# Optimization experiments

Measured on AMD Instinct MI355X. Metric: run time of the kernel, lower is better.

The kernel has to match this reference:

```python
import jax, jax.numpy as jnp
import numpy as np

LMAX = 3
D_IRREP = (LMAX + 1) ** 2  # 16
EPS = 1e-5


def _conv1d(x, w, pad):
    # x: [N, C_in, L], w: [C_out, C_in, K] -> [N, C_out, L]
    return jax.lax.conv_general_dilated(
        x, w, window_strides=(1,), padding=[(pad, pad)],
        dimension_numbers=("NCH", "OIH", "NCH"))


def setup_inputs() -> dict:
    key = jax.random.key(0)
    ks = jax.random.split(key, 8)
    B, Cin, Cout, N, K, RES = 128, 256, 256, 64, 5, 8
    return {
        "x": jax.random.normal(ks[0], (B, Cin * D_IRREP, N), jnp.float32),
        "weight": jax.random.normal(ks[1], (LMAX + 1, Cout, Cin, K), jnp.float32) / np.sqrt(Cin * K).astype(np.float32),
        "bias": jax.random.normal(ks[2], (1, 1, Cout), jnp.float32) * 0.02,
        "affine_weight": jnp.ones((LMAX + 1, Cout), jnp.float32),
        "gating_w": jax.random.normal(ks[3], (Cout, Cout), jnp.float32) / np.sqrt(Cout).astype(np.float32),
        "gating_b": jnp.zeros((Cout,), jnp.float32),
        "to_grid": jax.random.normal(ks[4], (RES, RES, D_IRREP), jnp.float32) * 0.3,
        "from_grid": jax.random.normal(ks[5], (RES, RES, D_IRREP), jnp.float32) * 0.3,
    }


def reference(x, weight, bias, affine_weight, gating_w, gating_b, to_grid, from_grid):
    B, CI, N = x.shape
    Cin = CI // D_IRREP
    Cout = weight.shape[1]
    pad = weight.shape[-1] // 2
    x = x.reshape(B, Cin, D_IRREP, N)

    # per-degree Conv1d over the time axis, irrep order folded into batch
    h_parts = []
    for l in range(LMAX + 1):
        lo, li = l * l, 2 * l + 1
        x_l = x[:, :, lo:lo + li, :]                                  # [B, Cin, li, N]
        x_l = x_l.transpose(0, 2, 1, 3).reshape(B * li, Cin, N)       # (b i) c n
        h_l = _conv1d(x_l, weight[l], pad)                            # [B*li, Cout, N]
        h_l = h_l.reshape(B, li, Cout, N).transpose(0, 3, 1, 2).reshape(B * N, li, Cout)  # (b n) i c
        if l == 0:
            h_l = h_l + bias
        h_parts.append(h_l)
    h = jnp.concatenate(h_parts, axis=1)                              # [B*N, 16, Cout]

    # rms_norm_sh: center l=0 over channels, degree-balanced RMS, per-degree affine
    degrees = np.repeat(np.arange(LMAX + 1), 2 * np.arange(LMAX + 1) + 1)  # [16]
    bal = jnp.asarray((1.0 / (2.0 * degrees + 1.0)) / (LMAX + 1), h.dtype)  # [16]
    mean0 = jnp.mean(h[:, :1, :], axis=2, keepdims=True)
    h = jnp.concatenate([h[:, :1, :] - mean0, h[:, 1:, :]], axis=1)
    var = jnp.einsum("zic,i->zc", h * h, bal)                         # [Z, C]
    inv = jax.lax.rsqrt(jnp.mean(var, axis=-1)[:, None, None] + EPS)  # [Z,1,1]
    h = h * inv * affine_weight[degrees][None]                        # [Z,16,C]

    # SeparableS2Activation: SiLU-gated scalars + S2 grid activation for l>0
    gate = jax.nn.silu(h[:, :1, :] @ gating_w.T + gating_b)           # [Z,1,C]
    grid = jax.nn.silu(jnp.einsum("bai,zic->zbac", to_grid, h))       # [Z,8,8,C]
    s2 = jnp.einsum("bai,zbac->zic", from_grid, grid)                 # [Z,16,C]
    h = jnp.concatenate([gate, s2[:, 1:, :]], axis=1)

    # (b n) i c -> b (c i) n
    out = h.reshape(B, N, D_IRREP, Cout).transpose(0, 3, 2, 1).reshape(B, Cout * D_IRREP, N)
    return out
```

## Files before the change

kernel.cpp:

```cpp
#include <hip/hip_runtime.h>
#include <hip/hip_bf16.h>

#define BB    128
#define CIN   256
#define COUT  256
#define NN    64
#define KW    5
#define DIRR  16
#define ZTOT  (BB*NN)
#define SX    264

typedef __attribute__((ext_vector_type(4))) float f32x4;
typedef __attribute__((ext_vector_type(8))) short s16x8;

__device__ inline ushort f2bf(float f) {
    __hip_bfloat16 h = __float2bfloat16(f);
    return *(const ushort*)&h;
}
__device__ inline float bf2f(ushort u) {
    union { unsigned int ui; float f; } cv; cv.ui = ((unsigned int)u) << 16;
    return cv.f;
}
__device__ inline float wave_sum(float v) {
    #pragma unroll
    for (int o = 32; o > 0; o >>= 1) v += __shfl_down(v, o, 64);
    return v;
}
__device__ inline float silu(float x) { return x / (1.f + __expf(-x)); }

__global__ __launch_bounds__(256) void pack_all_k(const float* __restrict__ w,
                                                  const float* __restrict__ gw,
                                                  const float* __restrict__ tg,
                                                  const float* __restrict__ fg,
                                                  ushort* __restrict__ wb,
                                                  ushort* __restrict__ gwb,
                                                  ushort* __restrict__ tgb,
                                                  ushort* __restrict__ fgTb)
{
    int idx = blockIdx.x * 256 + threadIdx.x;
    if (idx < 1310720) {
        int cl = idx & 31;
        int c  = (idx >> 5) & 255;
        int ch = (idx >> 13) & 7;
        int k  = (idx >> 16) % 5;
        int l  = idx / 327680;
        int cin = ch * 32 + cl;
        wb[idx] = f2bf(w[(((size_t)(l * COUT + c) * CIN) + cin) * KW + k]);
        return;
    }
    int j2 = idx - 1310720;
    if (j2 < 65536) {
        gwb[j2] = f2bf(gw[j2]);
    } else if (j2 < 66560) {
        int j = j2 - 65536;
        tgb[j] = f2bf(tg[j]);
    } else if (j2 < 67584) {
        int j = j2 - 66560;
        int p = j >> 4, i = j & 15;
        fgTb[i * 64 + p] = f2bf(fg[j]);
    }
}

__global__ __launch_bounds__(256, 3) void conv_mfma_k(const float* __restrict__ x,
                                                      const ushort* __restrict__ wb,
                                                      const float* __restrict__ bias,
                                                      ushort* __restrict__ hbuf)
{
    __shared__ __align__(16) ushort xs[68 * SX];

    const int tid  = threadIdx.x;
    const int lane = tid & 63;
    const int wid  = tid >> 6;
    const int blk  = blockIdx.x;
    const int b = blk >> 4, i = blk & 15;
    const int l = (i == 0) ? 0 : (i < 4) ? 1 : (i < 9) ? 2 : 3;

    {
        const float4* xb = (const float4*)(x + (((size_t)b * CIN) * DIRR + i) * NN);
        #pragma unroll
        for (int p = 0; p < 16; ++p) {
            int cin = (tid & 63) | ((p & 3) << 6);
            int nq  = ((tid >> 6) << 2) | (p >> 2);
            float4 v = xb[(size_t)cin * (DIRR * NN / 4) + nq];
            ushort* dst = xs + (size_t)(2 + nq * 4) * SX + cin;
            dst[0]      = f2bf(v.x);
            dst[SX]     = f2bf(v.y);
            dst[2 * SX] = f2bf(v.z);
            dst[3 * SX] = f2bf(v.w);
        }
        xs[ 0 * SX + tid] = 0; xs[ 1 * SX + tid] = 0;
        xs[66 * SX + tid] = 0; xs[67 * SX + tid] = 0;
    }
    __syncthreads();

    f32x4 acc[4][4];
    #pragma unroll
    for (int m = 0; m < 4; ++m)
        #pragma unroll
        for (int j = 0; j < 4; ++j) acc[m][j] = (f32x4){0.f, 0.f, 0.f, 0.f};

    const int kb = lane >> 4;
    const int lr = lane & 15;

    const ushort* wl = wb + (size_t)l * (40 * 8192);
    int boffB[4];
    #pragma unroll
    for (int j = 0; j < 4; ++j)
        boffB[j] = (wid * 64 + j * 16 + lr) * 32 + kb * 8;

    const ushort* arow = xs + (size_t)lr * SX + kb * 8;

#define LOADB(dst, t) do {                                              \
        const ushort* bt_ = wl + ((size_t)(t) << 13);                   \
        _Pragma("unroll")                                               \
        for (int j_ = 0; j_ < 4; ++j_)                                  \
            dst[j_] = *(const s16x8*)(bt_ + boffB[j_]);                 \
    } while (0)

#define MSTEP(bv, t) do {                                               \
        const ushort* ab_ = arow + (size_t)((t) >> 3) * SX + ((t) & 7) * 32; \
        s16x8 av_[4];                                                   \
        _Pragma("unroll")                                               \
        for (int m_ = 0; m_ < 4; ++m_)                                  \
            av_[m_] = *(const s16x8*)(ab_ + (size_t)m_ * 16 * SX);      \
        _Pragma("unroll")                                               \
        for (int m_ = 0; m_ < 4; ++m_) {                                \
            _Pragma("unroll")                                           \
            for (int j_ = 0; j_ < 4; ++j_)                              \
                acc[m_][j_] = __builtin_amdgcn_mfma_f32_16x16x32_bf16(  \
                    av_[m_], bv[j_], acc[m_][j_], 0, 0, 0);             \
        }                                                               \
    } while (0)

    s16x8 bv0[4], bv1[4], bv2[4], bv3[4];
    LOADB(bv0, 0);
    LOADB(bv1, 1);
    LOADB(bv2, 2);

    #pragma unroll 1
    for (int t = 0; t < 40; t += 4) {
        LOADB(bv3, t + 3);
        MSTEP(bv0, t);
        if (t + 4 < 40) LOADB(bv0, t + 4);
        MSTEP(bv1, t + 1);
        if (t + 5 < 40) LOADB(bv1, t + 5);
        MSTEP(bv2, t + 2);
        if (t + 6 < 40) LOADB(bv2, t + 6);
        MSTEP(bv3, t + 3);
    }
#undef LOADB
#undef MSTEP

    const int row0 = (lane >> 4) * 4;
    #pragma unroll
    for (int j = 0; j < 4; ++j) {
        int c = wid * 64 + j * 16 + lr;
        float bvv = (i == 0) ? bias[c] : 0.f;
        #pragma unroll
        for (int m = 0; m < 4; ++m)
            #pragma unroll
            for (int r = 0; r < 4; ++r) {
                int n = m * 16 + row0 + r;
                size_t z = (size_t)b * NN + n;
                hbuf[(z * DIRR + i) * COUT + c] = f2bf(acc[m][j][r] + bvv);
            }
    }
}

__global__ __launch_bounds__(256) void norm_k(const ushort* __restrict__ hbuf,
                                              const float* __restrict__ afw,
                                              ushort* __restrict__ hn2,
                                              ushort* __restrict__ hn0)
{
    __shared__ float red[16];
    const int z0 = blockIdx.x * 4;
    const int c = threadIdx.x;
    const int lane = c & 63, w = c >> 6;

    float hv[4][16];
    #pragma unroll
    for (int zz = 0; zz < 4; ++zz)
        #pragma unroll
        for (int i = 0; i < 16; ++i)
            hv[zz][i] = bf2f(hbuf[((size_t)(z0 + zz) * DIRR + i) * COUT + c]);

    float s[4];
    #pragma unroll
    for (int zz = 0; zz < 4; ++zz) s[zz] = wave_sum(hv[zz][0]);
    if (lane == 0) {
        #pragma unroll
        for (int zz = 0; zz < 4; ++zz) red[zz * 4 + w] = s[zz];
    }
    __syncthreads();
    #pragma unroll
    for (int zz = 0; zz < 4; ++zz) {
        float m = (red[zz * 4] + red[zz * 4 + 1] + red[zz * 4 + 2] + red[zz * 4 + 3]) * (1.f / 256.f);
        hv[zz][0] -= m;
    }

    const float bal[4] = {0.25f, 1.f / 12.f, 1.f / 20.f, 1.f / 28.f};
    float var[4];
    #pragma unroll
    for (int zz = 0; zz < 4; ++zz) {
        float v = bal[0] * hv[zz][0] * hv[zz][0];
        #pragma unroll
        for (int i = 1; i < 16; ++i) {
            int li = (i < 4) ? 1 : (i < 9) ? 2 : 3;
            v += bal[li] * hv[zz][i] * hv[zz][i];
        }
        var[zz] = wave_sum(v);
    }
    __syncthreads();
    if (lane == 0) {
        #pragma unroll
        for (int zz = 0; zz < 4; ++zz) red[zz * 4 + w] = var[zz];
    }
    __syncthreads();
    float inv[4];
    #pragma unroll
    for (int zz = 0; zz < 4; ++zz)
        inv[zz] = rsqrtf((red[zz * 4] + red[zz * 4 + 1] + red[zz * 4 + 2] + red[zz * 4 + 3]) * (1.f / 256.f) + 1e-5f);

    float a0 = afw[c], a1 = afw[COUT + c], a2 = afw[2 * COUT + c], a3 = afw[3 * COUT + c];
    #pragma unroll
    for (int zz = 0; zz < 4; ++zz) {
        s16x8 o0, o1;
        #pragma unroll
        for (int i = 0; i < 16; ++i) {
            float al = (i == 0) ? a0 : (i < 4) ? a1 : (i < 9) ? a2 : a3;
            ushort ub = f2bf(hv[zz][i] * inv[zz] * al);
            if (i < 8) o0[i] = (short)ub; else o1[i - 8] = (short)ub;
        }
        ushort* dst = hn2 + ((size_t)c * ZTOT + z0 + zz) * DIRR;
        *(s16x8*)dst = o0;
        *(s16x8*)(dst + 8) = o1;
        hn0[(size_t)(z0 + zz) * COUT + c] = (ushort)(unsigned short)o0[0];
    }
}

__global__ __launch_bounds__(256) void gate_k(const ushort* __restrict__ hn0,
                                              const ushort* __restrict__ gwb,
                                              const float* __restrict__ gb,
                                              float* __restrict__ out)
{
    const int b = blockIdx.x;
    const int tid = threadIdx.x;
    const int lane = tid & 63, w = tid >> 6;
    const int lr = lane & 15, kb = lane >> 4;

    f32x4 acc[4][4];
    #pragma unroll
    for (int m = 0; m < 4; ++m)
        #pragma unroll
        for (int n = 0; n < 4; ++n) acc[m][n] = (f32x4){0.f, 0.f, 0.f, 0.f};

    #pragma unroll 1
    for (int ks = 0; ks < 8; ++ks) {
        s16x8 av[4], bv[4];
        #pragma unroll
        for (int m = 0; m < 4; ++m)
            av[m] = *(const s16x8*)(hn0 + ((size_t)(b * 64 + m * 16 + lr) * 256 + ks * 32 + kb * 8));
        #pragma unroll
        for (int n = 0; n < 4; ++n)
            bv[n] = *(const s16x8*)(gwb + ((size_t)(w * 64 + n * 16 + lr) * 256 + ks * 32 + kb * 8));
        #pragma unroll
        for (int m = 0; m < 4; ++m)
            #pragma unroll
            for (int n = 0; n < 4; ++n)
                acc[m][n] = __builtin_amdgcn_mfma_f32_16x16x32_bf16(av[m], bv[n], acc[m][n], 0, 0, 0);
    }

    #pragma unroll
    for (int n = 0; n < 4; ++n) {
        int c = w * 64 + n * 16 + lr;
        float gbc = gb[c];
        #pragma unroll
        for (int m = 0; m < 4; ++m)
            #pragma unroll
            for (int r = 0; r < 4; ++r) {
                int nrow = m * 16 + kb * 4 + r;
                out[((size_t)b * COUT + c) * (DIRR * NN) + nrow] = silu(acc[m][n][r] + gbc);
            }
    }
}

__global__ __launch_bounds__(256) void grid_k(const ushort* __restrict__ hn2,
                                              const ushort* __restrict__ tgb,
                                              const ushort* __restrict__ fgTb,
                                              float* __restrict__ out)
{
    __shared__ __align__(16) char lds[36864 + 2048 + 2304];
    ushort* P_s  = (ushort*)lds;
    float*  S_s  = (float*)lds;
    ushort* tg_s = (ushort*)(lds + 36864);
    ushort* fgT_s= (ushort*)(lds + 36864 + 2048);

    const int bid = blockIdx.x;
    const int c  = bid & 255;
    const int zt = bid >> 8;
    const int z0 = zt * 256;
    const int tid = threadIdx.x;
    const int lane = tid & 63, w = tid >> 6;
    const int lr = lane & 15, kb = lane >> 4;

    #pragma unroll
    for (int q = 0; q < 4; ++q) {
        int idx = q * 256 + tid;
        tg_s[idx] = tgb[idx];
        int i = idx >> 6, p = idx & 63;
        fgT_s[i * 72 + p] = fgTb[idx];
    }
    __syncthreads();

    f32x4 acc[4][4];
    #pragma unroll
    for (int m = 0; m < 4; ++m)
        #pragma unroll
        for (int n = 0; n < 4; ++n) acc[m][n] = (f32x4){0.f, 0.f, 0.f, 0.f};

    s16x8 bv[4];
    #pragma unroll
    for (int n = 0; n < 4; ++n)
        bv[n] = (kb < 2) ? *(const s16x8*)(tg_s + (n * 16 + lr) * 16 + kb * 8)
                         : (s16x8){0,0,0,0,0,0,0,0};
    #pragma unroll
    for (int m = 0; m < 4; ++m) {
        int zl = w * 64 + m * 16 + lr;
        s16x8 av = (kb < 2) ? *(const s16x8*)(hn2 + ((size_t)c * ZTOT + z0 + zl) * DIRR + kb * 8)
                            : (s16x8){0,0,0,0,0,0,0,0};
        #pragma unroll
        for (int n = 0; n < 4; ++n)
            acc[m][n] = __builtin_amdgcn_mfma_f32_16x16x32_bf16(av, bv[n], acc[m][n], 0, 0, 0);
    }

    #pragma unroll
    for (int m = 0; m < 4; ++m)
        #pragma unroll
        for (int n = 0; n < 4; ++n)
            #pragma unroll
            for (int r = 0; r < 4; ++r) {
                int zl = w * 64 + m * 16 + kb * 4 + r;
                int p  = n * 16 + lr;
                P_s[zl * 72 + p] = f2bf(silu(acc[m][n][r]));
            }

    f32x4 acc2[4];
    #pragma unroll
    for (int m = 0; m < 4; ++m) acc2[m] = (f32x4){0.f, 0.f, 0.f, 0.f};
    #pragma unroll
    for (int ks = 0; ks < 2; ++ks) {
        s16x8 bv2 = *(const s16x8*)(fgT_s + lr * 72 + ks * 32 + kb * 8);
        #pragma unroll
        for (int m = 0; m < 4; ++m) {
            s16x8 av2 = *(const s16x8*)(P_s + (w * 64 + m * 16 + lr) * 72 + ks * 32 + kb * 8);
            acc2[m] = __builtin_amdgcn_mfma_f32_16x16x32_bf16(av2, bv2, acc2[m], 0, 0, 0);
        }
    }

    __syncthreads();

    #pragma unroll
    for (int m = 0; m < 4; ++m)
        #pragma unroll
        for (int r = 0; r < 4; ++r) {
            int zl = w * 64 + m * 16 + kb * 4 + r;
            S_s[zl * 17 + lr] = acc2[m][r];
        }
    __syncthreads();

    const int bb = tid >> 6, n = tid & 63;
    const int b0 = zt * 4;
    const float* srow = S_s + (bb * 64 + n) * 17;
    float* obase = out + ((size_t)(b0 + bb) * COUT + c) * (DIRR * NN) + n;
    #pragma unroll
    for (int i = 1; i < 16; ++i)
        obase[i * NN] = srow[i];
}

__global__ __launch_bounds__(256) void post_k(const ushort* __restrict__ hbuf,
                                              const float* __restrict__ afw,
                                              const float* __restrict__ gw,
                                              const float* __restrict__ gb,
                                              const float* __restrict__ tg,
                                              const float* __restrict__ fg,
                                              float* __restrict__ out)
{
    __shared__ float h0s[COUT];
    __shared__ float red[4];
    __shared__ float tgs[64 * 16];
    __shared__ float fgs[64 * 16];

    int z = blockIdx.x;
    int c = threadIdx.x;
    int b = z >> 6, n = z & 63;
    int lane = c & 63, wid = c >> 6;

    for (int idx = c; idx < 1024; idx += 256) { tgs[idx] = tg[idx]; fgs[idx] = fg[idx]; }

    float hv[16];
    #pragma unroll
    for (int i = 0; i < 16; ++i)
        hv[i] = bf2f(hbuf[((size_t)z * DIRR + i) * COUT + c]);

    float s0 = wave_sum(hv[0]);
    if (lane == 0) red[wid] = s0;
    __syncthreads();
    float mean0 = (red[0] + red[1] + red[2] + red[3]) * (1.f / 256.f);
    hv[0] -= mean0;

    const float bal[4] = {0.25f, 1.f / 12.f, 1.f / 20.f, 1.f / 28.f};
    float var = bal[0] * hv[0] * hv[0];
    #pragma unroll
    for (int i = 1; i < 16; ++i) {
        int li = (i < 4) ? 1 : (i < 9) ? 2 : 3;
        var += bal[li] * hv[i] * hv[i];
    }
    float s1 = wave_sum(var);
    __syncthreads();
    if (lane == 0) red[wid] = s1;
    __syncthreads();
    float inv = rsqrtf((red[0] + red[1] + red[2] + red[3]) * (1.f / 256.f) + 1e-5f);

    float a0 = afw[c], a1 = afw[COUT + c], a2 = afw[2 * COUT + c], a3 = afw[3 * COUT + c];
    #pragma unroll
    for (int i = 0; i < 16; ++i) {
        float al = (i == 0) ? a0 : (i < 4) ? a1 : (i < 9) ? a2 : a3;
        hv[i] *= inv * al;
    }
    h0s[c] = hv[0];
    __syncthreads();

    float g = gb[c];
    const float4* gwr = (const float4*)(gw + (size_t)c * COUT);
    #pragma unroll 4
    for (int j = 0; j < 64; ++j) {
        float4 wv = gwr[j];
        g += h0s[4 * j] * wv.x + h0s[4 * j + 1] * wv.y + h0s[4 * j + 2] * wv.z + h0s[4 * j + 3] * wv.w;
    }
    float gate = silu(g);

    float s2a[16];
    #pragma unroll
    for (int i = 0; i < 16; ++i) s2a[i] = 0.f;
    #pragma unroll 1
    for (int p = 0; p < 64; ++p) {
        float gv = 0.f;
        #pragma unroll
        for (int i = 0; i < 16; ++i) gv += tgs[p * 16 + i] * hv[i];
        gv = silu(gv);
        #pragma unroll
        for (int i = 0; i < 16; ++i) s2a[i] += fgs[p * 16 + i] * gv;
    }

    float* ob = out + (size_t)b * COUT * DIRR * NN + (size_t)c * DIRR * NN + n;
    ob[0] = gate;
    #pragma unroll
    for (int i = 1; i < 16; ++i) ob[i * NN] = s2a[i];
}

extern "C" void kernel_launch(void* const* d_in, const int* in_sizes, int n_in,
                              void* d_out, int out_size, void* d_ws, size_t ws_size,
                              hipStream_t stream)
{
    const float* x    = (const float*)d_in[0];
    const float* w    = (const float*)d_in[1];
    const float* bias = (const float*)d_in[2];
    const float* afw  = (const float*)d_in[3];
    const float* gw   = (const float*)d_in[4];
    const float* gb   = (const float*)d_in[5];
    const float* tg   = (const float*)d_in[6];
    const float* fg   = (const float*)d_in[7];
    float* out = (float*)d_out;

    const size_t off_hbuf = 0;
    const size_t off_wb   = 67108864;
    const size_t off_hn2  = 69730304;
    const size_t off_hn0  = off_hn2 + 67108864;
    const size_t off_gwb  = off_hn0 + 4194304;
    const size_t off_tgb  = off_gwb + 131072;
    const size_t off_fgT  = off_tgb + 2048;
    const size_t need     = off_fgT + 2048;

    ushort* hbuf = (ushort*)((char*)d_ws + off_hbuf);
    ushort* wb   = (ushort*)((char*)d_ws + off_wb);

    if (ws_size >= need) {
        ushort* hn2  = (ushort*)((char*)d_ws + off_hn2);
        ushort* hn0  = (ushort*)((char*)d_ws + off_hn0);
        ushort* gwb  = (ushort*)((char*)d_ws + off_gwb);
        ushort* tgb  = (ushort*)((char*)d_ws + off_tgb);
        ushort* fgTb = (ushort*)((char*)d_ws + off_fgT);

        pack_all_k <<<5384, 256, 0, stream>>>(w, gw, tg, fg, wb, gwb, tgb, fgTb);
        conv_mfma_k<<<BB * DIRR, 256, 0, stream>>>(x, wb, bias, hbuf);
        norm_k     <<<ZTOT / 4, 256, 0, stream>>>(hbuf, afw, hn2, hn0);
        gate_k     <<<BB, 256, 0, stream>>>(hn0, gwb, gb, out);
        grid_k     <<<256 * (ZTOT / 256), 256, 0, stream>>>(hn2, tgb, fgTb, out);
    } else {
        pack_all_k <<<5120, 256, 0, stream>>>(w, gw, tg, fg, wb,
                                              (ushort*)((char*)d_ws + off_wb),
                                              (ushort*)((char*)d_ws + off_wb),
                                              (ushort*)((char*)d_ws + off_wb));
        conv_mfma_k<<<BB * DIRR, 256, 0, stream>>>(x, wb, bias, hbuf);
        post_k     <<<ZTOT, 256, 0, stream>>>(hbuf, afw, gw, gb, tg, fg, out);
    }
}
```

Before: 267.0 us.

## Switch conv GEMM to 32x32x16 bf16 MFMA with repacked weight layout

Replaces the 16x16x32 MFMA tiling in the conv kernel with 32x32x16 MFMAs, using 2x2 tiles of 32x32 per wave instead of 4x4 tiles of 16x16. The weight packing is changed to 16-wide input-channel chunks to match the new K step, and the epilogue index mapping is updated for the 32x32 accumulator layout. Fewer, larger MFMAs mean fewer A/B operand loads from LDS and global memory per FLOP. The occupancy hint rises from 3 to 4 blocks per CU, which may constrain registers.

Result: faster. 248.8 us (-6.8%).

```diff
diff --git a/kernel.cpp b/kernel.cpp
--- a/kernel.cpp
+++ b/kernel.cpp
@@ -10,8 +10,9 @@
 #define ZTOT  (BB*NN)
 #define SX    264
 
-typedef __attribute__((ext_vector_type(4))) float f32x4;
-typedef __attribute__((ext_vector_type(8))) short s16x8;
+typedef __attribute__((ext_vector_type(4)))  float f32x4;
+typedef __attribute__((ext_vector_type(16))) float f32x16;
+typedef __attribute__((ext_vector_type(8)))  short s16x8;
 
 __device__ inline ushort f2bf(float f) {
     __hip_bfloat16 h = __float2bfloat16(f);
@@ -39,12 +40,13 @@
 {
     int idx = blockIdx.x * 256 + threadIdx.x;
     if (idx < 1310720) {
-        int cl = idx & 31;
-        int c  = (idx >> 5) & 255;
-        int ch = (idx >> 13) & 7;
-        int k  = (idx >> 16) % 5;
-        int l  = idx / 327680;
-        int cin = ch * 32 + cl;
+        int cl16 = idx & 15;
+        int c    = (idx >> 4) & 255;
+        int ch   = (idx >> 12) & 15;
+        int lk   = idx >> 16;
+        int k    = lk % 5;
+        int l    = lk / 5;
+        int cin  = ch * 16 + cl16;
         wb[idx] = f2bf(w[(((size_t)(l * COUT + c) * CIN) + cin) * KW + k]);
         return;
     }
@@ -61,7 +63,7 @@
     }
 }
 
-__global__ __launch_bounds__(256, 3) void conv_mfma_k(const float* __restrict__ x,
+__global__ __launch_bounds__(256, 4) void conv_mfma_k(const float* __restrict__ x,
                                                       const ushort* __restrict__ wb,
                                                       const float* __restrict__ bias,
                                                       ushort* __restrict__ hbuf)
@@ -93,74 +95,70 @@
     }
     __syncthreads();
 
-    f32x4 acc[4][4];
-    #pragma unroll
-    for (int m = 0; m < 4; ++m)
-        #pragma unroll
-        for (int j = 0; j < 4; ++j) acc[m][j] = (f32x4){0.f, 0.f, 0.f, 0.f};
-
-    const int kb = lane >> 4;
-    const int lr = lane & 15;
-
-    const ushort* wl = wb + (size_t)l * (40 * 8192);
-    int boffB[4];
-    #pragma unroll
-    for (int j = 0; j < 4; ++j)
-        boffB[j] = (wid * 64 + j * 16 + lr) * 32 + kb * 8;
-
-    const ushort* arow = xs + (size_t)lr * SX + kb * 8;
+    f32x16 acc[2][2];
+    #pragma unroll
+    for (int m = 0; m < 2; ++m)
+        #pragma unroll
+        for (int j = 0; j < 2; ++j)
+            #pragma unroll
+            for (int r = 0; r < 16; ++r) acc[m][j][r] = 0.f;
+
+    const int l31 = lane & 31;
+    const int kh  = lane >> 5;
+
+    const ushort* wl = wb + (size_t)l * (80 * 4096);
+    int boffB[2];
+    #pragma unroll
+    for (int j = 0; j < 2; ++j)
+        boffB[j] = (wid * 64 + j * 32 + l31) * 16 + kh * 8;
+
+    const ushort* arow = xs + (size_t)l31 * SX + kh * 8;
 
 #define LOADB(dst, t) do {                                              \
-        const ushort* bt_ = wl + ((size_t)(t) << 13);                   \
-        _Pragma("unroll")                                               \
-        for (int j_ = 0; j_ < 4; ++j_)                                  \
-            dst[j_] = *(const s16x8*)(bt_ + boffB[j_]);                 \
+        const ushort* bt_ = wl + ((size_t)(t) << 12);                   \
+        dst##0 = *(const s16x8*)(bt_ + boffB[0]);                       \
+        dst##1 = *(const s16x8*)(bt_ + boffB[1]);                       \
     } while (0)
 
 #define MSTEP(bv, t) do {                                               \
-        const ushort* ab_ = arow + (size_t)((t) >> 3) * SX + ((t) & 7) * 32; \
-        s16x8 av_[4];                                                   \
-        _Pragma("unroll")                                               \
-        for (int m_ = 0; m_ < 4; ++m_)                                  \
-            av_[m_] = *(const s16x8*)(ab_ + (size_t)m_ * 16 * SX);      \
-        _Pragma("unroll")                                               \
-        for (int m_ = 0; m_ < 4; ++m_) {                                \
-            _Pragma("unroll")                                           \
-            for (int j_ = 0; j_ < 4; ++j_)                              \
-                acc[m_][j_] = __builtin_amdgcn_mfma_f32_16x16x32_bf16(  \
-                    av_[m_], bv[j_], acc[m_][j_], 0, 0, 0);             \
-        }                                                               \
+        const ushort* ab_ = arow + (size_t)((t) >> 4) * SX + ((t) & 15) * 16; \
+        s16x8 av0_ = *(const s16x8*)(ab_);                              \
+        s16x8 av1_ = *(const s16x8*)(ab_ + (size_t)32 * SX);            \
+        acc[0][0] = __builtin_amdgcn_mfma_f32_32x32x16_bf16(av0_, bv##0, acc[0][0], 0, 0, 0); \
+        acc[0][1] = __builtin_amdgcn_mfma_f32_32x32x16_bf16(av0_, bv##1, acc[0][1], 0, 0, 0); \
+        acc[1][0] = __builtin_amdgcn_mfma_f32_32x32x16_bf16(av1_, bv##0, acc[1][0], 0, 0, 0); \
+        acc[1][1] = __builtin_amdgcn_mfma_f32_32x32x16_bf16(av1_, bv##1, acc[1][1], 0, 0, 0); \
     } while (0)
 
-    s16x8 bv0[4], bv1[4], bv2[4], bv3[4];
-    LOADB(bv0, 0);
-    LOADB(bv1, 1);
-    LOADB(bv2, 2);
+    s16x8 s0_0, s0_1, s1_0, s1_1, s2_0, s2_1, s3_0, s3_1;
+    LOADB(s0_, 0);
+    LOADB(s1_, 1);
+    LOADB(s2_, 2);
+    LOADB(s3_, 3);
 
     #pragma unroll 1
-    for (int t = 0; t < 40; t += 4) {
-        LOADB(bv3, t + 3);
-        MSTEP(bv0, t);
-        if (t + 4 < 40) LOADB(bv0, t + 4);
-        MSTEP(bv1, t + 1);
-        if (t + 5 < 40) LOADB(bv1, t + 5);
-        MSTEP(bv2, t + 2);
-        if (t + 6 < 40) LOADB(bv2, t + 6);
-        MSTEP(bv3, t + 3);
+    for (int t = 0; t < 80; t += 4) {
+        MSTEP(s0_, t);
+        if (t + 4 < 80) LOADB(s0_, t + 4);
+        MSTEP(s1_, t + 1);
+        if (t + 5 < 80) LOADB(s1_, t + 5);
+        MSTEP(s2_, t + 2);
+        if (t + 6 < 80) LOADB(s2_, t + 6);
+        MSTEP(s3_, t + 3);
+        if (t + 7 < 80) LOADB(s3_, t + 7);
     }
 #undef LOADB
 #undef MSTEP
 
-    const int row0 = (lane >> 4) * 4;
-    #pragma unroll
-    for (int j = 0; j < 4; ++j) {
-        int c = wid * 64 + j * 16 + lr;
+    #pragma unroll
+    for (int j = 0; j < 2; ++j) {
+        int c = wid * 64 + j * 32 + l31;
         float bvv = (i == 0) ? bias[c] : 0.f;
         #pragma unroll
-        for (int m = 0; m < 4; ++m)
+        for (int m = 0; m < 2; ++m)
             #pragma unroll
-            for (int r = 0; r < 4; ++r) {
-                int n = m * 16 + row0 + r;
+            for (int r = 0; r < 16; ++r) {
+                int n = m * 32 + (r & 3) + 8 * (r >> 2) + 4 * kh;
                 size_t z = (size_t)b * NN + n;
                 hbuf[(z * DIRR + i) * COUT + c] = f2bf(acc[m][j][r] + bvv);
             }
```
